# Optimization experiments

Measured on AMD Instinct MI355X. Metric: run time of the kernel, lower is better.

## Reference

```python
import jax, jax.numpy as jnp
import numpy as np

E = 200_000   # number of edges (messages)
T = 500_000   # number of triplets
H = 128       # hidden_channels
B = 8         # num_bilinear
R = 6         # num_radial
S = 7         # num_spherical


def setup_inputs() -> dict:
    key = jax.random.key(0)
    ks = jax.random.split(key, 18)
    w = 0.05  # small init scale for numerical stability
    return {
        "x":   jax.random.normal(ks[0], (E, H), dtype=jnp.float32),
        "rbf": jax.random.normal(ks[1], (E, R), dtype=jnp.float32),
        "sbf": jax.random.normal(ks[2], (T, S * R), dtype=jnp.float32),
        "idx_kj": jax.random.randint(ks[3], (T,), 0, E),
        "idx_ji": jax.random.randint(ks[4], (T,), 0, E),
        # parameters (stored as [in, out] so we apply x @ w)
        "lin_rbf_w": jax.random.normal(ks[5], (R, H), dtype=jnp.float32) * w,
        "lin_sbf_w": jax.random.normal(ks[6], (S * R, B), dtype=jnp.float32) * w,
        "lin_kj_w": jax.random.normal(ks[7], (H, H), dtype=jnp.float32) * w,
        "lin_kj_b": jnp.zeros((H,), dtype=jnp.float32),
        "lin_ji_w": jax.random.normal(ks[8], (H, H), dtype=jnp.float32) * w,
        "lin_ji_b": jnp.zeros((H,), dtype=jnp.float32),
        "W": jax.random.normal(ks[9], (H, B, H), dtype=jnp.float32) * (2.0 / H),
        "before_w": jax.random.normal(ks[10], (1, 2, H, H), dtype=jnp.float32) * w,
        "before_b": jnp.zeros((1, 2, H), dtype=jnp.float32),
        "lin_w": jax.random.normal(ks[11], (H, H), dtype=jnp.float32) * w,
        "lin_b": jnp.zeros((H,), dtype=jnp.float32),
        "after_w": jax.random.normal(ks[12], (2, 2, H, H), dtype=jnp.float32) * w,
        "after_b": jnp.zeros((2, 2, H), dtype=jnp.float32),
    }


def _residual(h, w2, b2):
    # DimeNet ResidualLayer: h + act(lin2(act(lin1(h))))
    return h + jax.nn.silu(jax.nn.silu(h @ w2[0] + b2[0]) @ w2[1] + b2[1])


def reference(x, rbf, sbf, idx_kj, idx_ji,
              lin_rbf_w, lin_sbf_w, lin_kj_w, lin_kj_b,
              lin_ji_w, lin_ji_b, W,
              before_w, before_b, lin_w, lin_b, after_w, after_b):
    act = jax.nn.silu
    rbf_p = rbf @ lin_rbf_w                     # [E, H]
    sbf_p = sbf @ lin_sbf_w                     # [T, B]
    x_ji = act(x @ lin_ji_w + lin_ji_b)         # [E, H]
    x_kj = act(x @ lin_kj_w + lin_kj_b) * rbf_p # [E, H]
    g = x_kj[idx_kj]                            # gather -> [T, H]
    # bilinear: 'wj,wl,ijl->wi' with i,l=hidden, j=bilinear
    m = jnp.einsum('wj,wl,ijl->wi', sbf_p, g, W)  # [T, H]
    agg = jax.ops.segment_sum(m, idx_ji, num_segments=x.shape[0])  # [E, H]
    h = x_ji + agg
    for i in range(before_w.shape[0]):
        h = _residual(h, before_w[i], before_b[i])
    h = act(h @ lin_w + lin_b) + x
    for i in range(after_w.shape[0]):
        h = _residual(h, after_w[i], after_b[i])
    return h
```

## Files before the change

### kernel.cpp

```cpp
#include <hip/hip_runtime.h>

#define E_N 200000
#define T_N 500000

typedef __attribute__((ext_vector_type(8))) short bf16x8;
typedef __attribute__((ext_vector_type(4))) float f32x4;
typedef unsigned short u16;
typedef unsigned int u32;

#define SWZ(b) ((b) ^ ((((b) >> 8) & 7) << 4))

#define SYNC_DRAIN() do { asm volatile("s_waitcnt vmcnt(0)" ::: "memory"); __syncthreads(); } while (0)

__device__ __forceinline__ u16 f2bf(float f){
  u32 u = __float_as_uint(f);
  return (u16)((u + 0x7fffu + ((u >> 16) & 1u)) >> 16);
}
__device__ __forceinline__ float silu_f(float v){
  return __fdividef(v, 1.f + __expf(-v));
}
__device__ __forceinline__ void gl_lds16(const void* g, void* l){
  __builtin_amdgcn_global_load_lds((const __attribute__((address_space(1))) u32*)g,
                                   (__attribute__((address_space(3))) u32*)l, 16, 0, 0);
}
__device__ __forceinline__ bf16x8 scale8(uint4 g, float s){
  union { bf16x8 v; u32 u[4]; } aa;
  u32 gu[4] = { g.x, g.y, g.z, g.w };
  #pragma unroll
  for (int q = 0; q < 4; q++){
    float lo = __uint_as_float(gu[q] << 16) * s;
    float hi = __uint_as_float(gu[q] & 0xffff0000u) * s;
    asm("v_cvt_pk_bf16_f32 %0, %1, %2" : "=v"(aa.u[q]) : "v"(lo), "v"(hi));
  }
  return aa.v;
}

__device__ __forceinline__ void gemm_tile(const char* ldsA, const char* ldsB,
                                          int wv, int lane, f32x4 acc[8]){
  const int arow = wv*16 + (lane & 15);
  const int kof = (lane >> 4) << 3;
  #pragma unroll
  for (int kc = 0; kc < 4; kc++){
    const int kb = (kc*32 + kof)*2;
    bf16x8 a = *(const bf16x8*)(ldsA + SWZ(arow*256 + kb));
    #pragma unroll
    for (int n = 0; n < 8; n++){
      bf16x8 b = *(const bf16x8*)(ldsB + SWZ((n*16 + (lane & 15))*256 + kb));
      acc[n] = __builtin_amdgcn_mfma_f32_16x16x32_bf16(a, b, acc[n], 0, 0, 0);
    }
  }
}

__global__ __launch_bounds__(256) void k_cvt_W(const float* __restrict__ W, u16* __restrict__ out){
  int i = blockIdx.x*256 + threadIdx.x;
  out[i] = f2bf(W[i]);
}

__global__ __launch_bounds__(256) void k_cvt_T(const float* __restrict__ jiw, const float* __restrict__ kjw,
                                               const float* __restrict__ bw, const float* __restrict__ lw,
                                               const float* __restrict__ aw, u16* __restrict__ out){
  int i = blockIdx.x*256 + threadIdx.x;
  int m = i >> 14, o = i & 16383;
  int n = o >> 7, k = o & 127;
  const float* src;
  switch (m){
    case 0: src = jiw; break;
    case 1: src = kjw; break;
    case 2: src = bw; break;
    case 3: src = bw + 16384; break;
    case 4: src = lw; break;
    default: src = aw + (m - 5)*16384; break;
  }
  out[i] = f2bf(src[k*128 + n]);
}

__global__ __launch_bounds__(256) void k_edge(const float* __restrict__ x, const float* __restrict__ rbf,
    const float* __restrict__ rbfw, const u16* __restrict__ wji, const u16* __restrict__ wkj,
    const float* __restrict__ bji, const float* __restrict__ bkj,
    float* __restrict__ out, u16* __restrict__ xkj)
{
  __shared__ __align__(16) char ldsA[16384];
  __shared__ __align__(16) char ldsB[32768];
  __shared__ float lrbf[64*6];
  __shared__ float lrbfw[6*128];
  __shared__ float lbj[128];
  __shared__ float lbk[128];
  const int tid = threadIdx.x;
  const int e0 = blockIdx.x * 64;

  #pragma unroll
  for (int it = 0; it < 4; it++){
    int i = it*256 + tid;
    int row = i >> 4, c8 = (i & 15) << 3;
    const float4* s = (const float4*)(x + (e0 + row)*128 + c8);
    float4 v0 = s[0], v1 = s[1];
    union { u16 us[8]; uint4 q; } u;
    u.us[0]=f2bf(v0.x); u.us[1]=f2bf(v0.y); u.us[2]=f2bf(v0.z); u.us[3]=f2bf(v0.w);
    u.us[4]=f2bf(v1.x); u.us[5]=f2bf(v1.y); u.us[6]=f2bf(v1.z); u.us[7]=f2bf(v1.w);
    *(uint4*)(ldsA + SWZ(row*256 + c8*2)) = u.q;
  }
  #pragma unroll
  for (int it = 0; it < 8; it++){
    int p = (it*256 + tid)*16;
    int pb = __builtin_amdgcn_readfirstlane(p);
    int n = p >> 8, o = p & 255;
    gl_lds16((const char*)wji + n*256 + (o ^ ((n & 7) << 4)), ldsB + pb);
  }
  for (int i = tid; i < 384; i += 256) lrbf[i] = rbf[e0*6 + i];
  for (int i = tid; i < 768; i += 256) lrbfw[i] = rbfw[i];
  if (tid < 128){ lbj[tid] = bji[tid]; lbk[tid] = bkj[tid]; }
  SYNC_DRAIN();

  const int wv = tid >> 6, lane = tid & 63;
  const int colb = lane & 15, rgrp = (lane >> 4) << 2;
  f32x4 acc[8];
  #pragma unroll
  for (int n = 0; n < 8; n++)
    #pragma unroll
    for (int r = 0; r < 4; r++) acc[n][r] = 0.f;
  gemm_tile(ldsA, ldsB, wv, lane, acc);
  #pragma unroll
  for (int n = 0; n < 8; n++){
    int col = n*16 + colb;
    float b = lbj[col];
    #pragma unroll
    for (int r = 0; r < 4; r++){
      int row = e0 + wv*16 + rgrp + r;
      out[row*128 + col] = silu_f(acc[n][r] + b);
    }
  }
  __syncthreads();
  #pragma unroll
  for (int it = 0; it < 8; it++){
    int p = (it*256 + tid)*16;
    int pb = __builtin_amdgcn_readfirstlane(p);
    int n = p >> 8, o = p & 255;
    gl_lds16((const char*)wkj + n*256 + (o ^ ((n & 7) << 4)), ldsB + pb);
  }
  SYNC_DRAIN();
  #pragma unroll
  for (int n = 0; n < 8; n++)
    #pragma unroll
    for (int r = 0; r < 4; r++) acc[n][r] = 0.f;
  gemm_tile(ldsA, ldsB, wv, lane, acc);

  float rb[4][6];
  #pragma unroll
  for (int r = 0; r < 4; r++)
    #pragma unroll
    for (int c = 0; c < 6; c++) rb[r][c] = lrbf[(wv*16 + rgrp + r)*6 + c];
  #pragma unroll
  for (int n = 0; n < 8; n++){
    int col = n*16 + colb;
    float b = lbk[col];
    float wc[6];
    #pragma unroll
    for (int c = 0; c < 6; c++) wc[c] = lrbfw[c*128 + col];
    #pragma unroll
    for (int r = 0; r < 4; r++){
      float rp = 0.f;
      #pragma unroll
      for (int c = 0; c < 6; c++) rp += rb[r][c]*wc[c];
      int row = e0 + wv*16 + rgrp + r;
      xkj[row*128 + col] = f2bf(silu_f(acc[n][r] + b) * rp);
    }
  }
}

__device__ __forceinline__ void stage_Wslice(const u16* __restrict__ Wbf, int j, char* dst, int tid){
  #pragma unroll
  for (int it = 0; it < 4; it++){
    int p = (it*512 + tid)*16;
    int pb = __builtin_amdgcn_readfirstlane(p);
    int n = p >> 8, o = p & 255;
    gl_lds16((const char*)Wbf + n*2048 + j*256 + (o ^ ((n & 7) << 4)), dst + pb);
  }
}

__global__ __launch_bounds__(512, 4) void k_trip(
    const u16* __restrict__ xkj, const float* __restrict__ sbf, const float* __restrict__ sbfw,
    const int* __restrict__ idx_kj, const int* __restrict__ idx_ji, const u16* __restrict__ Wbf,
    float* __restrict__ out)
{
  __shared__ __align__(16) char ldsW[2][32768];
  __shared__ float lss[256*8];
  __shared__ float lsw[336];
  __shared__ int lji[256];
  __shared__ int lkj[256];
  const int tid = threadIdx.x;
  const int t0 = blockIdx.x * 256;

  {
    float* scr = (float*)ldsW;
    for (int i = tid; i < 256*42; i += 512){
      int gi = t0*42 + i;
      scr[i] = (gi < T_N*42) ? sbf[gi] : 0.f;
    }
  }
  for (int i = tid; i < 336; i += 512) lsw[i] = sbfw[i];
  if (tid < 256){
    int w = t0 + tid;
    lji[tid] = (w < T_N) ? idx_ji[w] : -1;
    lkj[tid] = (w < T_N) ? idx_kj[w] : 0;
  }
  __syncthreads();

  const int wv = tid >> 6, lane = tid & 63;
  const int r15 = lane & 15, q = lane >> 4;

  uint4 graw[8];
  #pragma unroll
  for (int rt = 0; rt < 2; rt++){
    int row = lkj[wv*32 + rt*16 + r15];
    const char* src = (const char*)xkj + (long)row*256 + q*16;
    #pragma unroll
    for (int kc = 0; kc < 4; kc++)
      graw[rt*4 + kc] = *(const uint4*)(src + kc*64);
  }
  if (tid < 256){
    const float* scr = (const float*)ldsW;
    float a[8];
    #pragma unroll
    for (int k = 0; k < 8; k++) a[k] = 0.f;
    for (int c = 0; c < 42; c++){
      float v = scr[tid*42 + c];
      #pragma unroll
      for (int k = 0; k < 8; k++) a[k] += v * lsw[c*8 + k];
    }
    #pragma unroll
    for (int k = 0; k < 8; k++) lss[tid*8 + k] = a[k];
  }
  __syncthreads();
  stage_Wslice(Wbf, 0, ldsW[0], tid);
  SYNC_DRAIN();

  f32x4 acc0[8], acc1[8];
  #pragma unroll
  for (int n = 0; n < 8; n++)
    #pragma unroll
    for (int r = 0; r < 4; r++){ acc0[n][r] = 0.f; acc1[n][r] = 0.f; }

  const int swz_lane = (r15 & 7) << 4;
  for (int j = 0; j < 8; j++){
    const char* bp = ldsW[j & 1];
    if (j < 7) stage_Wslice(Wbf, j + 1, ldsW[(j + 1) & 1], tid);
    const float s0 = lss[(wv*32 + r15)*8 + j];
    const float s1 = lss[(wv*32 + 16 + r15)*8 + j];
    #pragma unroll
    for (int kc = 0; kc < 4; kc++){
      const int ab = (r15*256 + q*16 + kc*64) ^ swz_lane;
      bf16x8 aa0 = scale8(graw[kc], s0);
      bf16x8 aa1 = scale8(graw[4 + kc], s1);
      #pragma unroll
      for (int n = 0; n < 8; n++){
        bf16x8 b = *(const bf16x8*)(bp + n*4096 + ab);
        acc0[n] = __builtin_amdgcn_mfma_f32_16x16x32_bf16(aa0, b, acc0[n], 0, 0, 0);
        acc1[n] = __builtin_amdgcn_mfma_f32_16x16x32_bf16(aa1, b, acc1[n], 0, 0, 0);
      }
    }
    SYNC_DRAIN();
  }

  const int rgrp = q << 2;
  #pragma unroll
  for (int n = 0; n < 8; n++){
    const int col = n*16 + r15;
    #pragma unroll
    for (int r = 0; r < 4; r++){
      int e0i = lji[wv*32 + rgrp + r];
      if (e0i >= 0) unsafeAtomicAdd(out + e0i*128 + col, acc0[n][r]);
      int e1i = lji[wv*32 + 16 + rgrp + r];
      if (e1i >= 0) unsafeAtomicAdd(out + e1i*128 + col, acc1[n][r]);
    }
  }
}

__global__ __launch_bounds__(256) void k_epi(
    const float* __restrict__ x, float* __restrict__ hio, const u16* __restrict__ wm,
    const float* __restrict__ bb2, const float* __restrict__ linb, const float* __restrict__ ab2)
{
  __shared__ __align__(16) char ldsA[16384];
  __shared__ __align__(16) char ldsB[32768];
  __shared__ float lbias[7][128];
  const int tid = threadIdx.x;
  const int e0 = blockIdx.x * 64;
  if (tid < 128){
    lbias[0][tid] = bb2[tid];
    lbias[1][tid] = bb2[128 + tid];
    lbias[2][tid] = linb[tid];
    lbias[3][tid] = ab2[tid];
    lbias[4][tid] = ab2[128 + tid];
    lbias[5][tid] = ab2[256 + tid];
    lbias[6][tid] = ab2[384 + tid];
  }
  const int wv = tid >> 6, lane = tid & 63;
  const int colb = lane & 15, rgrp = (lane >> 4) << 2;
  float h[8][4], t[8][4];
  f32x4 acc[8];
  #pragma unroll
  for (int n = 0; n < 8; n++)
    #pragma unroll
    for (int r = 0; r < 4; r++)
      h[n][r] = hio[(e0 + wv*16 + rgrp + r)*128 + n*16 + colb];

#define STAGE_B(mi) { \
  _Pragma("unroll") \
  for (int it = 0; it < 8; it++){ \
    int p = (it*256 + tid)*16; \
    int pb = __builtin_amdgcn_readfirstlane(p); \
    int nn = p >> 8, o = p & 255; \
    gl_lds16((const char*)wm + (mi)*32768 + nn*256 + (o ^ ((nn & 7) << 4)), ldsB + pb); \
  } }
#define WRITE_A(v) { \
  _Pragma("unroll") \
  for (int n = 0; n < 8; n++){ \
    _Pragma("unroll") \
    for (int r = 0; r < 4; r++){ \
      int rowl = wv*16 + rgrp + r; \
      *(u16*)(ldsA + SWZ(rowl*256 + (n*16 + colb)*2)) = f2bf(v[n][r]); \
    } } }
#define RUN_GEMM() { \
  _Pragma("unroll") \
  for (int n = 0; n < 8; n++){ \
    _Pragma("unroll") \
    for (int r = 0; r < 4; r++) acc[n][r] = 0.f; } \
  gemm_tile(ldsA, ldsB, wv, lane, acc); }

  STAGE_B(0); WRITE_A(h); SYNC_DRAIN(); RUN_GEMM();
  #pragma unroll
  for (int n = 0; n < 8; n++){ float b = lbias[0][n*16 + colb];
    #pragma unroll
    for (int r = 0; r < 4; r++) t[n][r] = silu_f(acc[n][r] + b); }
  __syncthreads(); STAGE_B(1); WRITE_A(t); SYNC_DRAIN(); RUN_GEMM();
  #pragma unroll
  for (int n = 0; n < 8; n++){ float b = lbias[1][n*16 + colb];
    #pragma unroll
    for (int r = 0; r < 4; r++) h[n][r] += silu_f(acc[n][r] + b); }
  __syncthreads(); STAGE_B(2); WRITE_A(h); SYNC_DRAIN(); RUN_GEMM();
  #pragma unroll
  for (int n = 0; n < 8; n++){ float b = lbias[2][n*16 + colb];
    #pragma unroll
    for (int r = 0; r < 4; r++)
      h[n][r] = silu_f(acc[n][r] + b) + x[(e0 + wv*16 + rgrp + r)*128 + n*16 + colb]; }
  __syncthreads(); STAGE_B(3); WRITE_A(h); SYNC_DRAIN(); RUN_GEMM();
  #pragma unroll
  for (int n = 0; n < 8; n++){ float b = lbias[3][n*16 + colb];
    #pragma unroll
    for (int r = 0; r < 4; r++) t[n][r] = silu_f(acc[n][r] + b); }
  __syncthreads(); STAGE_B(4); WRITE_A(t); SYNC_DRAIN(); RUN_GEMM();
  #pragma unroll
  for (int n = 0; n < 8; n++){ float b = lbias[4][n*16 + colb];
    #pragma unroll
    for (int r = 0; r < 4; r++) h[n][r] += silu_f(acc[n][r] + b); }
  __syncthreads(); STAGE_B(5); WRITE_A(h); SYNC_DRAIN(); RUN_GEMM();
  #pragma unroll
  for (int n = 0; n < 8; n++){ float b = lbias[5][n*16 + colb];
    #pragma unroll
    for (int r = 0; r < 4; r++) t[n][r] = silu_f(acc[n][r] + b); }
  __syncthreads(); STAGE_B(6); WRITE_A(t); SYNC_DRAIN(); RUN_GEMM();
  #pragma unroll
  for (int n = 0; n < 8; n++){ float b = lbias[6][n*16 + colb];
    #pragma unroll
    for (int r = 0; r < 4; r++) h[n][r] += silu_f(acc[n][r] + b); }

  #pragma unroll
  for (int n = 0; n < 8; n++)
    #pragma unroll
    for (int r = 0; r < 4; r++)
      hio[(e0 + wv*16 + rgrp + r)*128 + n*16 + colb] = h[n][r];
#undef STAGE_B
#undef WRITE_A
#undef RUN_GEMM
}

extern "C" void kernel_launch(void* const* d_in, const int* in_sizes, int n_in,
                              void* d_out, int out_size, void* d_ws, size_t ws_size,
                              hipStream_t stream)
{
  const float* x    = (const float*)d_in[0];
  const float* rbf  = (const float*)d_in[1];
  const float* sbf  = (const float*)d_in[2];
  const int* idx_kj = (const int*)d_in[3];
  const int* idx_ji = (const int*)d_in[4];
  const float* rbfw = (const float*)d_in[5];
  const float* sbfw = (const float*)d_in[6];
  const float* kjw  = (const float*)d_in[7];
  const float* kjb  = (const float*)d_in[8];
  const float* jiw  = (const float*)d_in[9];
  const float* jib  = (const float*)d_in[10];
  const float* W    = (const float*)d_in[11];
  const float* bw   = (const float*)d_in[12];
  const float* bb   = (const float*)d_in[13];
  const float* lw   = (const float*)d_in[14];
  const float* lb   = (const float*)d_in[15];
  const float* aw   = (const float*)d_in[16];
  const float* ab   = (const float*)d_in[17];
  float* out = (float*)d_out;
  char* ws = (char*)d_ws;
  u16* Wbf  = (u16*)(ws);
  u16* linT = (u16*)(ws + 262144);
  u16* xkj  = (u16*)(ws + 1048576);

  k_cvt_W<<<dim3(512), dim3(256), 0, stream>>>(W, Wbf);
  k_cvt_T<<<dim3(576), dim3(256), 0, stream>>>(jiw, kjw, bw, lw, aw, linT);
  k_edge<<<dim3(E_N/64), dim3(256), 0, stream>>>(x, rbf, rbfw, linT, linT + 16384, jib, kjb, out, xkj);
  k_trip<<<dim3((T_N + 255)/256), dim3(512), 0, stream>>>(xkj, sbf, sbfw, idx_kj, idx_ji, Wbf, out);
  k_epi<<<dim3(E_N/64), dim3(256), 0, stream>>>(x, out, linT + 2*16384, bb, lb, ab);
}
```

Measured before the change: 680.7 us.

## Scatter triplet messages with packed bf16 atomics into separate buffer

The triplet kernel's scatter-add now accumulates into a separate zero-initialised bf16 buffer using packed bf16x2 global atomics, built from lane-pair shuffles, instead of one fp32 atomic per element into the output. The epilogue adds this bf16 aggregate to the fp32 x_ji values it loads. The goal is to halve the number of atomic operations and the bytes they move. The cost is an extra zeroing kernel, an extra buffer read, and bf16 rounding during accumulation, which can reduce accuracy. The last barrier in the W-slice loop is also dropped.

```diff
diff --git a/kernel.cpp b/kernel.cpp
--- a/kernel.cpp
+++ b/kernel.cpp
@@ -49,6 +49,12 @@
       acc[n] = __builtin_amdgcn_mfma_f32_16x16x32_bf16(a, b, acc[n], 0, 0, 0);
     }
   }
+}
+
+__global__ __launch_bounds__(256) void k_zero(uint4* __restrict__ p, int n16){
+  int stride = gridDim.x * 256;
+  for (int i = blockIdx.x*256 + threadIdx.x; i < n16; i += stride)
+    p[i] = make_uint4(0u, 0u, 0u, 0u);
 }
 
 __global__ __launch_bounds__(256) void k_cvt_W(const float* __restrict__ W, u16* __restrict__ out){
@@ -177,10 +183,11 @@
   }
 }
 
+template<int PK>
 __global__ __launch_bounds__(512, 4) void k_trip(
     const u16* __restrict__ xkj, const float* __restrict__ sbf, const float* __restrict__ sbfw,
     const int* __restrict__ idx_kj, const int* __restrict__ idx_ji, const u16* __restrict__ Wbf,
-    float* __restrict__ out)
+    float* __restrict__ out, u16* __restrict__ agg)
 {
   __shared__ __align__(16) char ldsW[2][32768];
   __shared__ float lss[256*8];
@@ -258,25 +265,48 @@
         acc1[n] = __builtin_amdgcn_mfma_f32_16x16x32_bf16(aa1, b, acc1[n], 0, 0, 0);
       }
     }
-    SYNC_DRAIN();
+    if (j < 7) SYNC_DRAIN();
   }
 
   const int rgrp = q << 2;
-  #pragma unroll
-  for (int n = 0; n < 8; n++){
-    const int col = n*16 + r15;
-    #pragma unroll
-    for (int r = 0; r < 4; r++){
-      int e0i = lji[wv*32 + rgrp + r];
-      if (e0i >= 0) unsafeAtomicAdd(out + e0i*128 + col, acc0[n][r]);
-      int e1i = lji[wv*32 + 16 + rgrp + r];
-      if (e1i >= 0) unsafeAtomicAdd(out + e1i*128 + col, acc1[n][r]);
-    }
-  }
-}
-
+  if (PK){
+    const bool ev = (r15 & 1) == 0;
+    #pragma unroll
+    for (int n = 0; n < 8; n++){
+      const int colp = n*16 + (r15 & ~1);
+      #pragma unroll
+      for (int r = 0; r < 4; r++){
+        float v0 = acc0[n][r];
+        float p0 = __shfl_xor(v0, 1);
+        float v1 = acc1[n][r];
+        float p1 = __shfl_xor(v1, 1);
+        int e = lji[wv*32 + (ev ? 0 : 16) + rgrp + r];
+        u32 pkv = ev ? ((u32)f2bf(v0) | ((u32)f2bf(p0) << 16))
+                     : ((u32)f2bf(p1) | ((u32)f2bf(v1) << 16));
+        u16* ad = agg + (size_t)e*128 + colp;
+        if (e >= 0)
+          asm volatile("global_atomic_pk_add_bf16 %0, %1, off" :: "v"(ad), "v"(pkv) : "memory");
+      }
+    }
+  } else {
+    #pragma unroll
+    for (int n = 0; n < 8; n++){
+      const int col = n*16 + r15;
+      #pragma unroll
+      for (int r = 0; r < 4; r++){
+        int e0i = lji[wv*32 + rgrp + r];
+        if (e0i >= 0) unsafeAtomicAdd(out + e0i*128 + col, acc0[n][r]);
+        int e1i = lji[wv*32 + 16 + rgrp + r];
+        if (e1i >= 0) unsafeAtomicAdd(out + e1i*128 + col, acc1[n][r]);
+      }
+    }
+  }
+}
+
+template<int MERGE>
 __global__ __launch_bounds__(256) void k_epi(
-    const float* __restrict__ x, float* __restrict__ hio, const u16* __restrict__ wm,
+    const float* __restrict__ x, float* __restrict__ hio, const u16* __restrict__ agg,
+    const u16* __restrict__ wm,
     const float* __restrict__ bb2, const float* __restrict__ linb, const float* __restrict__ ab2)
 {
   __shared__ __align__(16) char ldsA[16384];
@@ -300,8 +330,12 @@
   #pragma unroll
   for (int n = 0; n < 8; n++)
     #pragma unroll
-    for (int r = 0; r < 4; r++)
-      h[n][r] = hio[(e0 + wv*16 + rgrp + r)*128 + n*16 + colb];
+    for (int r = 0; r < 4; r++){
+      int idx = (e0 + wv*16 + rgrp + r)*128 + n*16 + colb;
+      float v = hio[idx];
+      if (MERGE) v += __uint_as_float(((u32)agg[idx]) << 16);
+      h[n][r] = v;
+    }
 
 #define STAGE_B(mi) { \
   _Pragma("unroll") \
@@ -400,10 +434,21 @@
   u16* Wbf  = (u16*)(ws);
   u16* linT = (u16*)(ws + 262144);
   u16* xkj  = (u16*)(ws + 1048576);
+  const size_t agg_off = 1048576 + (size_t)E_N*128*2;
+  u16* agg  = (u16*)(ws + agg_off);
+  const size_t need = agg_off + (size_t)E_N*128*2;
+  const bool pk = (ws_size >= need);
 
   k_cvt_W<<<dim3(512), dim3(256), 0, stream>>>(W, Wbf);
   k_cvt_T<<<dim3(576), dim3(256), 0, stream>>>(jiw, kjw, bw, lw, aw, linT);
+  if (pk)
+    k_zero<<<dim3(2048), dim3(256), 0, stream>>>((uint4*)agg, E_N*128*2/16);
   k_edge<<<dim3(E_N/64), dim3(256), 0, stream>>>(x, rbf, rbfw, linT, linT + 16384, jib, kjb, out, xkj);
-  k_trip<<<dim3((T_N + 255)/256), dim3(512), 0, stream>>>(xkj, sbf, sbfw, idx_kj, idx_ji, Wbf, out);
-  k_epi<<<dim3(E_N/64), dim3(256), 0, stream>>>(x, out, linT + 2*16384, bb, lb, ab);
-}
+  if (pk){
+    k_trip<1><<<dim3((T_N + 255)/256), dim3(512), 0, stream>>>(xkj, sbf, sbfw, idx_kj, idx_ji, Wbf, out, agg);
+    k_epi<1><<<dim3(E_N/64), dim3(256), 0, stream>>>(x, out, agg, linT + 2*16384, bb, lb, ab);
+  } else {
+    k_trip<0><<<dim3((T_N + 255)/256), dim3(512), 0, stream>>>(xkj, sbf, sbfw, idx_kj, idx_ji, Wbf, out, agg);
+    k_epi<0><<<dim3(E_N/64), dim3(256), 0, stream>>>(x, out, agg, linT + 2*16384, bb, lb, ab);
+  }
+}
```

After: 720.7 us. 5.9% more time.

## Replace atomic scatter with CSR sort-by-destination and gather in epilogue

Applied to the files above, without the earlier changes.

Builds a CSR index of triplets grouped by idx_ji (histogram, three-pass scan, fill) on every call. The triplet kernel then writes per-triplet messages as bf16 to a buffer instead of issuing float atomics. The epilogue gathers and sums each edge's messages before its MLP chain. This removes 64M float atomics to global memory, at the cost of a 128MB intermediate write and read, extra launches, bf16 rounding of the messages, and a dependence on workspace size. The path falls back to atomics if the workspace is too small.

```diff
diff --git a/kernel.cpp b/kernel.cpp
--- a/kernel.cpp
+++ b/kernel.cpp
@@ -2,6 +2,7 @@
 
 #define E_N 200000
 #define T_N 500000
+#define NB_SCAN 196
 
 typedef __attribute__((ext_vector_type(8))) short bf16x8;
 typedef __attribute__((ext_vector_type(4))) float f32x4;
@@ -16,6 +17,9 @@
   u32 u = __float_as_uint(f);
   return (u16)((u + 0x7fffu + ((u >> 16) & 1u)) >> 16);
 }
+__device__ __forceinline__ float bf2f(u16 v){
+  return __uint_as_float(((u32)v) << 16);
+}
 __device__ __forceinline__ float silu_f(float v){
   return __fdividef(v, 1.f + __expf(-v));
 }
@@ -51,11 +55,78 @@
   }
 }
 
+__global__ __launch_bounds__(256) void k_zero32(u32* __restrict__ p, int n){
+  int stride = gridDim.x * 256;
+  for (int i = blockIdx.x*256 + threadIdx.x; i < n; i += stride) p[i] = 0u;
+}
+__global__ __launch_bounds__(256) void k_hist(const int* __restrict__ idx, u32* __restrict__ counts){
+  int i = blockIdx.x*256 + threadIdx.x;
+  if (i < T_N) atomicAdd(&counts[idx[i]], 1u);
+}
+__global__ __launch_bounds__(1024) void k_scanA(const u32* __restrict__ counts, u32* __restrict__ bsum){
+  __shared__ u32 red[16];
+  int b = blockIdx.x, t = threadIdx.x, i = b*1024 + t;
+  u32 v = (i < E_N) ? counts[i] : 0u;
+  #pragma unroll
+  for (int off = 1; off < 64; off <<= 1) v += __shfl_xor(v, off);
+  if ((t & 63) == 0) red[t >> 6] = v;
+  __syncthreads();
+  if (t == 0){
+    u32 s = 0;
+    #pragma unroll
+    for (int k = 0; k < 16; k++) s += red[k];
+    bsum[b] = s;
+  }
+}
+__global__ __launch_bounds__(256) void k_scanB(const u32* __restrict__ bsum, u32* __restrict__ boff){
+  __shared__ u32 wsum[4];
+  int t = threadIdx.x, lane = t & 63, wv = t >> 6;
+  u32 v = (t < NB_SCAN) ? bsum[t] : 0u;
+  u32 x = v;
+  #pragma unroll
+  for (int off = 1; off < 64; off <<= 1){
+    u32 y = __shfl_up(x, off);
+    if (lane >= off) x += y;
+  }
+  if (lane == 63) wsum[wv] = x;
+  __syncthreads();
+  u32 wo = 0;
+  for (int k = 0; k < wv; k++) wo += wsum[k];
+  if (t < NB_SCAN) boff[t] = wo + x - v;
+}
+__global__ __launch_bounds__(1024) void k_scanC(const u32* __restrict__ counts, const u32* __restrict__ boff,
+                                                u32* __restrict__ rowstart, u32* __restrict__ cursor){
+  __shared__ u32 wsum[16];
+  int b = blockIdx.x, t = threadIdx.x, i = b*1024 + t;
+  int lane = t & 63, wv = t >> 6;
+  u32 v = (i < E_N) ? counts[i] : 0u;
+  u32 x = v;
+  #pragma unroll
+  for (int off = 1; off < 64; off <<= 1){
+    u32 y = __shfl_up(x, off);
+    if (lane >= off) x += y;
+  }
+  if (lane == 63) wsum[wv] = x;
+  __syncthreads();
+  u32 wo = 0;
+  for (int k = 0; k < wv; k++) wo += wsum[k];
+  u32 ex = boff[b] + wo + x - v;
+  if (i < E_N){ rowstart[i] = ex; cursor[i] = ex; }
+  if (i == E_N - 1) rowstart[E_N] = ex + v;
+}
+__global__ __launch_bounds__(256) void k_fill(const int* __restrict__ idx, u32* __restrict__ cursor,
+                                              u32* __restrict__ order){
+  int i = blockIdx.x*256 + threadIdx.x;
+  if (i < T_N){
+    u32 p = atomicAdd(&cursor[idx[i]], 1u);
+    order[p] = i;
+  }
+}
+
 __global__ __launch_bounds__(256) void k_cvt_W(const float* __restrict__ W, u16* __restrict__ out){
   int i = blockIdx.x*256 + threadIdx.x;
   out[i] = f2bf(W[i]);
 }
-
 __global__ __launch_bounds__(256) void k_cvt_T(const float* __restrict__ jiw, const float* __restrict__ kjw,
                                                const float* __restrict__ bw, const float* __restrict__ lw,
                                                const float* __restrict__ aw, u16* __restrict__ out){
@@ -177,10 +248,11 @@
   }
 }
 
+template<int CSR>
 __global__ __launch_bounds__(512, 4) void k_trip(
     const u16* __restrict__ xkj, const float* __restrict__ sbf, const float* __restrict__ sbfw,
     const int* __restrict__ idx_kj, const int* __restrict__ idx_ji, const u16* __restrict__ Wbf,
-    float* __restrict__ out)
+    float* __restrict__ out, u16* __restrict__ mbuf)
 {
   __shared__ __align__(16) char ldsW[2][32768];
   __shared__ float lss[256*8];
@@ -200,7 +272,7 @@
   for (int i = tid; i < 336; i += 512) lsw[i] = sbfw[i];
   if (tid < 256){
     int w = t0 + tid;
-    lji[tid] = (w < T_N) ? idx_ji[w] : -1;
+    if (!CSR) lji[tid] = (w < T_N) ? idx_ji[w] : -1;
     lkj[tid] = (w < T_N) ? idx_kj[w] : 0;
   }
   __syncthreads();
@@ -258,30 +330,52 @@
         acc1[n] = __builtin_amdgcn_mfma_f32_16x16x32_bf16(aa1, b, acc1[n], 0, 0, 0);
       }
     }
-    SYNC_DRAIN();
+    if (j < 7) SYNC_DRAIN();
   }
 
   const int rgrp = q << 2;
-  #pragma unroll
-  for (int n = 0; n < 8; n++){
-    const int col = n*16 + r15;
-    #pragma unroll
-    for (int r = 0; r < 4; r++){
-      int e0i = lji[wv*32 + rgrp + r];
-      if (e0i >= 0) unsafeAtomicAdd(out + e0i*128 + col, acc0[n][r]);
-      int e1i = lji[wv*32 + 16 + rgrp + r];
-      if (e1i >= 0) unsafeAtomicAdd(out + e1i*128 + col, acc1[n][r]);
-    }
-  }
-}
-
+  if (CSR){
+    const bool ev = (r15 & 1) == 0;
+    #pragma unroll
+    for (int n = 0; n < 8; n++){
+      const int colb2 = (n*16 + (r15 & ~1))*2;
+      #pragma unroll
+      for (int r = 0; r < 4; r++){
+        float v0 = acc0[n][r], p0 = __shfl_xor(v0, 1);
+        float v1 = acc1[n][r], p1 = __shfl_xor(v1, 1);
+        int row = wv*32 + (ev ? 0 : 16) + rgrp + r;
+        u32 pk = ev ? ((u32)f2bf(v0) | ((u32)f2bf(p0) << 16))
+                    : ((u32)f2bf(p1) | ((u32)f2bf(v1) << 16));
+        if (t0 + row < T_N)
+          *(u32*)((char*)mbuf + (size_t)(t0 + row)*256 + colb2) = pk;
+      }
+    }
+  } else {
+    #pragma unroll
+    for (int n = 0; n < 8; n++){
+      const int col = n*16 + r15;
+      #pragma unroll
+      for (int r = 0; r < 4; r++){
+        int e0i = lji[wv*32 + rgrp + r];
+        if (e0i >= 0) unsafeAtomicAdd(out + e0i*128 + col, acc0[n][r]);
+        int e1i = lji[wv*32 + 16 + rgrp + r];
+        if (e1i >= 0) unsafeAtomicAdd(out + e1i*128 + col, acc1[n][r]);
+      }
+    }
+  }
+}
+
+template<int CSR>
 __global__ __launch_bounds__(256) void k_epi(
-    const float* __restrict__ x, float* __restrict__ hio, const u16* __restrict__ wm,
+    const float* __restrict__ x, float* __restrict__ hio,
+    const u32* __restrict__ rowstart, const u32* __restrict__ order, const u16* __restrict__ mbuf,
+    const u16* __restrict__ wm,
     const float* __restrict__ bb2, const float* __restrict__ linb, const float* __restrict__ ab2)
 {
   __shared__ __align__(16) char ldsA[16384];
   __shared__ __align__(16) char ldsB[32768];
   __shared__ float lbias[7][128];
+  __shared__ u32 lrs[65];
   const int tid = threadIdx.x;
   const int e0 = blockIdx.x * 64;
   if (tid < 128){
@@ -293,6 +387,7 @@
     lbias[5][tid] = ab2[256 + tid];
     lbias[6][tid] = ab2[384 + tid];
   }
+  if (CSR && tid < 65) lrs[tid] = rowstart[e0 + tid];
   const int wv = tid >> 6, lane = tid & 63;
   const int colb = lane & 15, rgrp = (lane >> 4) << 2;
   float h[8][4], t[8][4];
@@ -302,6 +397,20 @@
     #pragma unroll
     for (int r = 0; r < 4; r++)
       h[n][r] = hio[(e0 + wv*16 + rgrp + r)*128 + n*16 + colb];
+
+  if (CSR){
+    __syncthreads();
+    #pragma unroll
+    for (int r = 0; r < 4; r++){
+      u32 rs = lrs[wv*16 + rgrp + r], re = lrs[wv*16 + rgrp + r + 1];
+      for (u32 d = rs; d < re; ++d){
+        const u16* mrow = mbuf + (size_t)order[d]*128;
+        #pragma unroll
+        for (int n = 0; n < 8; n++)
+          h[n][r] += bf2f(mrow[n*16 + colb]);
+      }
+    }
+  }
 
 #define STAGE_B(mi) { \
   _Pragma("unroll") \
@@ -396,14 +505,37 @@
   const float* aw   = (const float*)d_in[16];
   const float* ab   = (const float*)d_in[17];
   float* out = (float*)d_out;
-  char* ws = (char*)d_ws;
-  u16* Wbf  = (u16*)(ws);
-  u16* linT = (u16*)(ws + 262144);
-  u16* xkj  = (u16*)(ws + 1048576);
+  char* p = (char*)d_ws;
+
+  u16* Wbf  = (u16*)p;
+  u16* linT = (u16*)(p + 262144);
+  u16* xkj  = (u16*)(p + (1 << 20));
+  size_t o = (1 << 20) + (size_t)E_N*256;
+  u32* counts   = (u32*)(p + o);  o += (size_t)E_N*4;
+  u32* cursor   = (u32*)(p + o);  o += (size_t)E_N*4;
+  u32* rowstart = (u32*)(p + o);  o += (size_t)(E_N + 1)*4 + 60;
+  u32* bsum     = (u32*)(p + o);  o += 1024;
+  u32* boff     = (u32*)(p + o);  o += 1024;
+  u32* order    = (u32*)(p + o);  o += (size_t)T_N*4;
+  u16* mbuf     = (u16*)(p + o);  o += (size_t)T_N*256;
+  const bool csr = (ws_size >= o);
 
   k_cvt_W<<<dim3(512), dim3(256), 0, stream>>>(W, Wbf);
   k_cvt_T<<<dim3(576), dim3(256), 0, stream>>>(jiw, kjw, bw, lw, aw, linT);
+  if (csr){
+    k_zero32<<<dim3(256), dim3(256), 0, stream>>>(counts, E_N);
+    k_hist<<<dim3((T_N + 255)/256), dim3(256), 0, stream>>>(idx_ji, counts);
+    k_scanA<<<dim3(NB_SCAN), dim3(1024), 0, stream>>>(counts, bsum);
+    k_scanB<<<dim3(1), dim3(256), 0, stream>>>(bsum, boff);
+    k_scanC<<<dim3(NB_SCAN), dim3(1024), 0, stream>>>(counts, boff, rowstart, cursor);
+    k_fill<<<dim3((T_N + 255)/256), dim3(256), 0, stream>>>(idx_ji, cursor, order);
+  }
   k_edge<<<dim3(E_N/64), dim3(256), 0, stream>>>(x, rbf, rbfw, linT, linT + 16384, jib, kjb, out, xkj);
-  k_trip<<<dim3((T_N + 255)/256), dim3(512), 0, stream>>>(xkj, sbf, sbfw, idx_kj, idx_ji, Wbf, out);
-  k_epi<<<dim3(E_N/64), dim3(256), 0, stream>>>(x, out, linT + 2*16384, bb, lb, ab);
-}
+  if (csr){
+    k_trip<1><<<dim3((T_N + 255)/256), dim3(512), 0, stream>>>(xkj, sbf, sbfw, idx_kj, idx_ji, Wbf, out, mbuf);
+    k_epi<1><<<dim3(E_N/64), dim3(256), 0, stream>>>(x, out, rowstart, order, mbuf, linT + 2*16384, bb, lb, ab);
+  } else {
+    k_trip<0><<<dim3((T_N + 255)/256), dim3(512), 0, stream>>>(xkj, sbf, sbfw, idx_kj, idx_ji, Wbf, out, mbuf);
+    k_epi<0><<<dim3(E_N/64), dim3(256), 0, stream>>>(x, out, rowstart, order, mbuf, linT + 2*16384, bb, lb, ab);
+  }
+}
```

Measured after the change: 769.3 us. +13.0%, slower.

## Read bilinear W directly from global memory in triplet kernel, halve block size

Applied to the files above, without the earlier changes.

The triplet kernel no longer stages each W slice into double-buffered LDS with global_load_lds and per-slice barriers. Each lane now loads its B fragments straight from global memory, relying on L1/L2 caching of the small bf16 weight tensor. The block shrinks to 256 threads and 128 triplets, which frees LDS and removes the per-iteration syncs. The cost is many more global/cache loads sitting on the MFMA critical path, since every wave re-fetches W fragments without the swizzled LDS reuse.

```diff
diff --git a/kernel.cpp b/kernel.cpp
--- a/kernel.cpp
+++ b/kernel.cpp
@@ -55,7 +55,6 @@
   int i = blockIdx.x*256 + threadIdx.x;
   out[i] = f2bf(W[i]);
 }
-
 __global__ __launch_bounds__(256) void k_cvt_T(const float* __restrict__ jiw, const float* __restrict__ kjw,
                                                const float* __restrict__ bw, const float* __restrict__ lw,
                                                const float* __restrict__ aw, u16* __restrict__ out){
@@ -167,38 +166,25 @@
   }
 }
 
-__device__ __forceinline__ void stage_Wslice(const u16* __restrict__ Wbf, int j, char* dst, int tid){
-  #pragma unroll
-  for (int it = 0; it < 4; it++){
-    int p = (it*512 + tid)*16;
-    int pb = __builtin_amdgcn_readfirstlane(p);
-    int n = p >> 8, o = p & 255;
-    gl_lds16((const char*)Wbf + n*2048 + j*256 + (o ^ ((n & 7) << 4)), dst + pb);
-  }
-}
-
-__global__ __launch_bounds__(512, 4) void k_trip(
+__global__ __launch_bounds__(256, 3) void k_trip(
     const u16* __restrict__ xkj, const float* __restrict__ sbf, const float* __restrict__ sbfw,
     const int* __restrict__ idx_kj, const int* __restrict__ idx_ji, const u16* __restrict__ Wbf,
     float* __restrict__ out)
 {
-  __shared__ __align__(16) char ldsW[2][32768];
-  __shared__ float lss[256*8];
+  __shared__ float scr[128*42];
+  __shared__ float lss[128*8];
   __shared__ float lsw[336];
-  __shared__ int lji[256];
-  __shared__ int lkj[256];
+  __shared__ int lji[128];
+  __shared__ int lkj[128];
   const int tid = threadIdx.x;
-  const int t0 = blockIdx.x * 256;
-
-  {
-    float* scr = (float*)ldsW;
-    for (int i = tid; i < 256*42; i += 512){
-      int gi = t0*42 + i;
-      scr[i] = (gi < T_N*42) ? sbf[gi] : 0.f;
-    }
-  }
-  for (int i = tid; i < 336; i += 512) lsw[i] = sbfw[i];
-  if (tid < 256){
+  const int t0 = blockIdx.x * 128;
+
+  for (int i = tid; i < 128*42; i += 256){
+    long gi = (long)t0*42 + i;
+    scr[i] = (gi < (long)T_N*42) ? sbf[gi] : 0.f;
+  }
+  for (int i = tid; i < 336; i += 256) lsw[i] = sbfw[i];
+  if (tid < 128){
     int w = t0 + tid;
     lji[tid] = (w < T_N) ? idx_ji[w] : -1;
     lkj[tid] = (w < T_N) ? idx_kj[w] : 0;
@@ -217,8 +203,7 @@
     for (int kc = 0; kc < 4; kc++)
       graw[rt*4 + kc] = *(const uint4*)(src + kc*64);
   }
-  if (tid < 256){
-    const float* scr = (const float*)ldsW;
+  if (tid < 128){
     float a[8];
     #pragma unroll
     for (int k = 0; k < 8; k++) a[k] = 0.f;
@@ -231,8 +216,6 @@
     for (int k = 0; k < 8; k++) lss[tid*8 + k] = a[k];
   }
   __syncthreads();
-  stage_Wslice(Wbf, 0, ldsW[0], tid);
-  SYNC_DRAIN();
 
   f32x4 acc0[8], acc1[8];
   #pragma unroll
@@ -240,25 +223,23 @@
     #pragma unroll
     for (int r = 0; r < 4; r++){ acc0[n][r] = 0.f; acc1[n][r] = 0.f; }
 
-  const int swz_lane = (r15 & 7) << 4;
+  const char* wbase = (const char*)Wbf + (size_t)r15*2048 + (size_t)q*16;
   for (int j = 0; j < 8; j++){
-    const char* bp = ldsW[j & 1];
-    if (j < 7) stage_Wslice(Wbf, j + 1, ldsW[(j + 1) & 1], tid);
     const float s0 = lss[(wv*32 + r15)*8 + j];
     const float s1 = lss[(wv*32 + 16 + r15)*8 + j];
+    const char* wj = wbase + j*256;
     #pragma unroll
     for (int kc = 0; kc < 4; kc++){
-      const int ab = (r15*256 + q*16 + kc*64) ^ swz_lane;
       bf16x8 aa0 = scale8(graw[kc], s0);
       bf16x8 aa1 = scale8(graw[4 + kc], s1);
+      const char* wk = wj + kc*64;
       #pragma unroll
       for (int n = 0; n < 8; n++){
-        bf16x8 b = *(const bf16x8*)(bp + n*4096 + ab);
+        bf16x8 b = *(const bf16x8*)(wk + n*32768);
         acc0[n] = __builtin_amdgcn_mfma_f32_16x16x32_bf16(aa0, b, acc0[n], 0, 0, 0);
         acc1[n] = __builtin_amdgcn_mfma_f32_16x16x32_bf16(aa1, b, acc1[n], 0, 0, 0);
       }
     }
-    SYNC_DRAIN();
   }
 
   const int rgrp = q << 2;
@@ -268,9 +249,9 @@
     #pragma unroll
     for (int r = 0; r < 4; r++){
       int e0i = lji[wv*32 + rgrp + r];
-      if (e0i >= 0) unsafeAtomicAdd(out + e0i*128 + col, acc0[n][r]);
+      if (e0i >= 0) unsafeAtomicAdd(out + (size_t)e0i*128 + col, acc0[n][r]);
       int e1i = lji[wv*32 + 16 + rgrp + r];
-      if (e1i >= 0) unsafeAtomicAdd(out + e1i*128 + col, acc1[n][r]);
+      if (e1i >= 0) unsafeAtomicAdd(out + (size_t)e1i*128 + col, acc1[n][r]);
     }
   }
 }
@@ -404,6 +385,6 @@
   k_cvt_W<<<dim3(512), dim3(256), 0, stream>>>(W, Wbf);
   k_cvt_T<<<dim3(576), dim3(256), 0, stream>>>(jiw, kjw, bw, lw, aw, linT);
   k_edge<<<dim3(E_N/64), dim3(256), 0, stream>>>(x, rbf, rbfw, linT, linT + 16384, jib, kjb, out, xkj);
-  k_trip<<<dim3((T_N + 255)/256), dim3(512), 0, stream>>>(xkj, sbf, sbfw, idx_kj, idx_ji, Wbf, out);
+  k_trip<<<dim3((T_N + 127)/128), dim3(256), 0, stream>>>(xkj, sbf, sbfw, idx_kj, idx_ji, Wbf, out);
   k_epi<<<dim3(E_N/64), dim3(256), 0, stream>>>(x, out, linT + 2*16384, bb, lb, ab);
 }
```

After: 1.068 ms. +56.8%, slower.
